# Optimization experiments

Hardware: AMD Instinct MI355X
Metric: run time of the kernel (lower is better)

## Reference

```python
import jax, jax.numpy as jnp
import numpy as np
from jax import lax

B, T, LM, H = 16, 60, 63, 64   # batch, frames, landmark dim, lstm hidden
IMG_H, IMG_W = 240, 320
CONV_FEAT = 252                 # 4 * 7 * 9


def _conv(x, w, b, s):
    # x: [N, Cin, H, W], w: [Cout, Cin, kh, kw], VALID padding, stride s
    y = lax.conv_general_dilated(x, w, (s, s), 'VALID',
                                 dimension_numbers=('NCHW', 'OIHW', 'NCHW'))
    return y + b[None, :, None, None]


def setup_inputs() -> dict:
    key = jax.random.key(0)
    ks = jax.random.split(key, 24)
    s = 0.05
    d = {
        'input': jax.random.normal(ks[0], (B, T, LM), jnp.float32),
        'video': jax.random.uniform(ks[1], (B, T, IMG_H, IMG_W), jnp.float32),
        'W00': jax.random.normal(ks[2], (LM, LM), jnp.float32) * s,
        'b00': jnp.zeros((LM,), jnp.float32),
        'W01': jax.random.normal(ks[3], (64, LM), jnp.float32) * s,
        'b01': jnp.zeros((64,), jnp.float32),
        'Wc0': jax.random.normal(ks[4], (16, 1, 5, 5), jnp.float32) * s,
        'bc0': jnp.zeros((16,), jnp.float32),
        'Wc1': jax.random.normal(ks[5], (16, 16, 5, 5), jnp.float32) * s,
        'bc1': jnp.zeros((16,), jnp.float32),
        'Wc2': jax.random.normal(ks[6], (4, 16, 2, 2), jnp.float32) * s,
        'bc2': jnp.zeros((4,), jnp.float32),
        'Wih': jax.random.normal(ks[7], (4 * H, 64 + CONV_FEAT), jnp.float32) * s,
        'Whh': jax.random.normal(ks[8], (4 * H, H), jnp.float32) * s,
        'bih': jnp.zeros((4 * H,), jnp.float32),
        'bhh': jnp.zeros((4 * H,), jnp.float32),
        'W10': jax.random.normal(ks[9], (32, H), jnp.float32) * s,
        'b10': jnp.zeros((32,), jnp.float32),
        'W11': jax.random.normal(ks[10], (32, 32), jnp.float32) * s,
        'b11': jnp.zeros((32,), jnp.float32),
        'W12': jax.random.normal(ks[11], (256, 32), jnp.float32) * s,
        'b12': jnp.zeros((256,), jnp.float32),
    }
    return d


def reference(input, video, W00, b00, W01, b01, Wc0, bc0, Wc1, bc1, Wc2, bc2,
              Wih, Whh, bih, bhh, W10, b10, W11, b11, W12, b12):
    relu = jax.nn.relu
    # per-frame landmark MLP, vectorized over all frames: [B, T, 64]
    f = relu(jnp.einsum('btl,ml->btm', input, W00) + b00)
    f = relu(jnp.einsum('btl,ml->btm', f, W01) + b01)
    # per-frame conv features, all frames in one batched conv: [B*T, 1, 240, 320]
    v = video.reshape(B * T, 1, IMG_H, IMG_W)
    v = relu(_conv(v, Wc0, bc0, 4))          # [B*T, 16, 59, 79]
    v = relu(_conv(v, Wc1, bc1, 4))          # [B*T, 16, 14, 19]
    v = relu(_conv(v, Wc2, bc2, 2))          # [B*T, 4, 7, 9]
    v = v.reshape(B, T, CONV_FEAT)
    # frame inputs to LSTM: [B, T, 316]
    x = jnp.concatenate([f, v], axis=-1)
    # Torch semantics: LSTM called unbatched with 2D input [B, 316] per frame,
    # so the batch dim is consumed as a sequence; state carries across frames.
    # Total sequence is frame-major: [T, B, 316] -> [T*B, 316].
    seq = x.transpose(1, 0, 2).reshape(T * B, -1)

    def step(carry, xt):
        h, c = carry
        g = xt @ Wih.T + bih + h @ Whh.T + bhh
        i, fg, gg, o = jnp.split(g, 4)
        c = jax.nn.sigmoid(fg) * c + jax.nn.sigmoid(i) * jnp.tanh(gg)
        h = jax.nn.sigmoid(o) * jnp.tanh(c)
        return (h, c), h

    h0 = jnp.zeros((H,), seq.dtype)
    _, hs = lax.scan(step, (h0, h0), seq)    # [T*B, H]
    out = hs[-B:]                            # last frame's full output: [B, H]
    out = relu(out @ W10.T + b10)
    out = relu(out @ W11.T + b11)
    return out @ W12.T + b12                 # [B, 256]
```

## Files before the change

### kernel.cpp

```cpp
#include <hip/hip_runtime.h>
#include <math.h>

#define B_   16
#define T_   60
#define LMD  63
#define IH   240
#define IW   320
#define XDIM 316
#define NSEQ 960
#define NPROD 255

#define G_BYTES   983040

#define P_W0T   0
#define P_BAND  416
#define P_PART  6944
#define P_C1L   8236
#define P_XROW  12760
#define P_X0S   13076
#define P_F1S   13140
#define P_ACT   0
#define P_HSL   512
#define P_M1S   1536
#define P_M2S   1568
#define POOLN   20736

__device__ __forceinline__ float rl(float v, int k) {
    return __uint_as_float((unsigned)__builtin_amdgcn_readlane((int)__float_as_uint(v), k));
}
__device__ __forceinline__ float sig_f(float x) {
    return __builtin_amdgcn_rcpf(1.0f + __expf(-x));
}
__device__ __forceinline__ float tanh_f(float x) {
    return 1.0f - 2.0f * __builtin_amdgcn_rcpf(__expf(2.0f * x) + 1.0f);
}

__device__ __forceinline__ int ensure_rows(const int* flg, int R, int target, int l) {
    while (R < target) {
        int idx = R + l;
        int v = 1;
        if (idx < NSEQ)
            v = __hip_atomic_load(&flg[idx], __ATOMIC_ACQUIRE, __HIP_MEMORY_SCOPE_AGENT);
        unsigned long long m = __ballot(v != 0);
        if (m == 0xFFFFFFFFFFFFFFFFull) { R += 64; continue; }
        int n = (int)(__ffsll((long long)~m) - 1);
        if (n > 0) R += n;
        else __builtin_amdgcn_s_sleep(16);
    }
    return R;
}

__global__ void k_zero(int* __restrict__ flg) {
    int i = blockIdx.x * 256 + threadIdx.x;
    if (i < NSEQ) flg[i] = 0;
}

#define REPW(M) M(0) M(1) M(2) M(3) M(4) M(5) M(6) M(7) \
                M(8) M(9) M(10) M(11) M(12) M(13) M(14) M(15)

__global__ __launch_bounds__(256, 1) void k_all(
        const float* __restrict__ inp,  const float* __restrict__ video,
        const float* __restrict__ W00,  const float* __restrict__ b00,
        const float* __restrict__ W01,  const float* __restrict__ b01,
        const float* __restrict__ Wc0,  const float* __restrict__ bc0,
        const float* __restrict__ Wc1,  const float* __restrict__ bc1,
        const float* __restrict__ Wc2,  const float* __restrict__ bc2,
        const float* __restrict__ Wih,  const float* __restrict__ Whh,
        const float* __restrict__ bih,  const float* __restrict__ bhh,
        const float* __restrict__ W10,  const float* __restrict__ b10,
        const float* __restrict__ W11,  const float* __restrict__ b11,
        const float* __restrict__ W12,  const float* __restrict__ b12,
        float* __restrict__ G, int* __restrict__ flg, float* __restrict__ out)
{
    __shared__ __align__(16) float pool[POOLN];
    int tid = threadIdx.x;

    if (blockIdx.x != 0) {
        float* W0T  = pool + P_W0T;
        float* band = pool + P_BAND;
        float* part = pool + P_PART;
        float* c1L  = pool + P_C1L;
        float* xrow = pool + P_XROW;
        float* x0s  = pool + P_X0S;
        float* f1s  = pool + P_F1S;

        int ch1 = tid & 15, ic = tid >> 4;
        int wave = tid >> 6, lane = tid & 63;
        int d0 = tid / 79, c0c0 = tid % 79;
        int pos1 = tid + 256;
        bool has1 = (pos1 < 395);
        int d1 = has1 ? pos1 / 79 : 0, c0c1 = has1 ? pos1 % 79 : 0;

        for (int i = tid; i < 400; i += 256) { int ch = i / 25, tap = i % 25; W0T[tap * 16 + ch] = Wc0[i]; }
        if (tid < 16) W0T[25 * 16 + tid] = bc0[tid];
        float w1r[25];
#pragma unroll
        for (int tap = 0; tap < 25; ++tap)
            w1r[tap] = Wc1[(ch1 * 16 + ic) * 25 + tap];

        for (int s = (int)blockIdx.x - 1; s < NSEQ; s += NPROD) {
            int t = s >> 4, b = s & 15;
            int bt = b * T_ + t;
            const float* vid = video + (size_t)bt * (IH * IW);

            if (tid < LMD) x0s[tid] = inp[bt * LMD + tid];
            __syncthreads();
            if (tid < LMD) {
                const float* wr = W00 + tid * LMD;
                float a0 = 0.f, a1 = 0.f, a2 = 0.f, a3 = 0.f;
                for (int k = 0; k < 60; k += 4) {
                    a0 += x0s[k + 0] * wr[k + 0];
                    a1 += x0s[k + 1] * wr[k + 1];
                    a2 += x0s[k + 2] * wr[k + 2];
                    a3 += x0s[k + 3] * wr[k + 3];
                }
                a0 += x0s[60] * wr[60]; a1 += x0s[61] * wr[61]; a2 += x0s[62] * wr[62];
                f1s[tid] = fmaxf(((a0 + a1) + (a2 + a3)) + b00[tid], 0.f);
            }
            __syncthreads();
            if (tid < 64) {
                const float* wr = W01 + tid * LMD;
                float a0 = 0.f, a1 = 0.f, a2 = 0.f, a3 = 0.f;
                for (int k = 0; k < 60; k += 4) {
                    a0 += f1s[k + 0] * wr[k + 0];
                    a1 += f1s[k + 1] * wr[k + 1];
                    a2 += f1s[k + 2] * wr[k + 2];
                    a3 += f1s[k + 3] * wr[k + 3];
                }
                a0 += f1s[60] * wr[60]; a1 += f1s[61] * wr[61]; a2 += f1s[62] * wr[62];
                xrow[tid] = fmaxf(((a0 + a1) + (a2 + a3)) + b01[tid], 0.f);
            }

            float PX0[25], PX1[25];
            {
                const float* vb = vid + (4 * d0) * IW + c0c0 * 4;
#pragma unroll
                for (int kr = 0; kr < 5; ++kr) {
                    float4 v = *(const float4*)(vb + kr * IW);
                    PX0[kr*5+0]=v.x; PX0[kr*5+1]=v.y; PX0[kr*5+2]=v.z; PX0[kr*5+3]=v.w;
                    PX0[kr*5+4]=vb[kr*IW+4];
                }
                if (has1) {
                    const float* vc = vid + (4 * d1) * IW + c0c1 * 4;
#pragma unroll
                    for (int kr = 0; kr < 5; ++kr) {
                        float4 v = *(const float4*)(vc + kr * IW);
                        PX1[kr*5+0]=v.x; PX1[kr*5+1]=v.y; PX1[kr*5+2]=v.z; PX1[kr*5+3]=v.w;
                        PX1[kr*5+4]=vc[kr*IW+4];
                    }
                }
            }
            __syncthreads();

            for (int r1 = 0; r1 < 14; ++r1) {
                {
                    float acc[16];
                    {
                        const float4* b4 = (const float4*)&W0T[25 * 16];
                        float4 ba = b4[0], bb = b4[1], bc = b4[2], bd = b4[3];
                        acc[0]=ba.x; acc[1]=ba.y; acc[2]=ba.z; acc[3]=ba.w;
                        acc[4]=bb.x; acc[5]=bb.y; acc[6]=bb.z; acc[7]=bb.w;
                        acc[8]=bc.x; acc[9]=bc.y; acc[10]=bc.z; acc[11]=bc.w;
                        acc[12]=bd.x; acc[13]=bd.y; acc[14]=bd.z; acc[15]=bd.w;
                    }
#pragma unroll
                    for (int tap = 0; tap < 25; ++tap) {
                        float p = PX0[tap];
                        const float4* w4 = (const float4*)&W0T[tap * 16];
                        float4 wa = w4[0], wb = w4[1], wc = w4[2], wd = w4[3];
                        acc[0]+=p*wa.x; acc[1]+=p*wa.y; acc[2]+=p*wa.z; acc[3]+=p*wa.w;
                        acc[4]+=p*wb.x; acc[5]+=p*wb.y; acc[6]+=p*wb.z; acc[7]+=p*wb.w;
                        acc[8]+=p*wc.x; acc[9]+=p*wc.y; acc[10]+=p*wc.z; acc[11]+=p*wc.w;
                        acc[12]+=p*wd.x; acc[13]+=p*wd.y; acc[14]+=p*wd.z; acc[15]+=p*wd.w;
                    }
#pragma unroll
                    for (int ch = 0; ch < 16; ++ch)
                        band[ch * 408 + d0 * 80 + c0c0] = fmaxf(acc[ch], 0.f);
                }
                if (has1) {
                    float acc[16];
                    {
                        const float4* b4 = (const float4*)&W0T[25 * 16];
                        float4 ba = b4[0], bb = b4[1], bc = b4[2], bd = b4[3];
                        acc[0]=ba.x; acc[1]=ba.y; acc[2]=ba.z; acc[3]=ba.w;
                        acc[4]=bb.x; acc[5]=bb.y; acc[6]=bb.z; acc[7]=bb.w;
                        acc[8]=bc.x; acc[9]=bc.y; acc[10]=bc.z; acc[11]=bc.w;
                        acc[12]=bd.x; acc[13]=bd.y; acc[14]=bd.z; acc[15]=bd.w;
                    }
#pragma unroll
                    for (int tap = 0; tap < 25; ++tap) {
                        float p = PX1[tap];
                        const float4* w4 = (const float4*)&W0T[tap * 16];
                        float4 wa = w4[0], wb = w4[1], wc = w4[2], wd = w4[3];
                        acc[0]+=p*wa.x; acc[1]+=p*wa.y; acc[2]+=p*wa.z; acc[3]+=p*wa.w;
                        acc[4]+=p*wb.x; acc[5]+=p*wb.y; acc[6]+=p*wb.z; acc[7]+=p*wb.w;
                        acc[8]+=p*wc.x; acc[9]+=p*wc.y; acc[10]+=p*wc.z; acc[11]+=p*wc.w;
                        acc[12]+=p*wd.x; acc[13]+=p*wd.y; acc[14]+=p*wd.z; acc[15]+=p*wd.w;
                    }
#pragma unroll
                    for (int ch = 0; ch < 16; ++ch)
                        band[ch * 408 + d1 * 80 + c0c1] = fmaxf(acc[ch], 0.f);
                }

                if (r1 + 1 < 14) {
                    const float* vb = vid + (16 * (r1+1) + 4 * d0) * IW + c0c0 * 4;
#pragma unroll
                    for (int kr = 0; kr < 5; ++kr) {
                        float4 v = *(const float4*)(vb + kr * IW);
                        PX0[kr*5+0]=v.x; PX0[kr*5+1]=v.y; PX0[kr*5+2]=v.z; PX0[kr*5+3]=v.w;
                        PX0[kr*5+4]=vb[kr*IW+4];
                    }
                    if (has1) {
                        const float* vc = vid + (16 * (r1+1) + 4 * d1) * IW + c0c1 * 4;
#pragma unroll
                        for (int kr = 0; kr < 5; ++kr) {
                            float4 v = *(const float4*)(vc + kr * IW);
                            PX1[kr*5+0]=v.x; PX1[kr*5+1]=v.y; PX1[kr*5+2]=v.z; PX1[kr*5+3]=v.w;
                            PX1[kr*5+4]=vc[kr*IW+4];
                        }
                    }
                }
                __syncthreads();

                const float* bb0 = &band[ic * 408];
                for (int c1c = 0; c1c < 19; ++c1c) {
                    const float* bb = bb0 + c1c * 4;
                    float a0, a1, a2, a3, a4;
                    {
                        float4 v = *(const float4*)(bb);       float sc = bb[4];
                        a0 = v.x*w1r[0]  + v.y*w1r[1]  + v.z*w1r[2]  + v.w*w1r[3]  + sc*w1r[4];
                    }
                    {
                        float4 v = *(const float4*)(bb + 80);  float sc = bb[84];
                        a1 = v.x*w1r[5]  + v.y*w1r[6]  + v.z*w1r[7]  + v.w*w1r[8]  + sc*w1r[9];
                    }
                    {
                        float4 v = *(const float4*)(bb + 160); float sc = bb[164];
                        a2 = v.x*w1r[10] + v.y*w1r[11] + v.z*w1r[12] + v.w*w1r[13] + sc*w1r[14];
                    }
                    {
                        float4 v = *(const float4*)(bb + 240); float sc = bb[244];
                        a3 = v.x*w1r[15] + v.y*w1r[16] + v.z*w1r[17] + v.w*w1r[18] + sc*w1r[19];
                    }
                    {
                        float4 v = *(const float4*)(bb + 320); float sc = bb[324];
                        a4 = v.x*w1r[20] + v.y*w1r[21] + v.z*w1r[22] + v.w*w1r[23] + sc*w1r[24];
                    }
                    float p = ((a0 + a1) + (a2 + a3)) + a4;
                    p += __shfl_xor(p, 16);
                    p += __shfl_xor(p, 32);
                    if (lane < 16)
                        part[c1c * 68 + wave * 17 + ch1] = p;
                }
                __syncthreads();

                for (int o = tid; o < 304; o += 256) {
                    int c1c = o >> 4, ch = o & 15;
                    const float* pp = &part[c1c * 68 + ch];
                    float v = bc1[ch] + pp[0] + pp[17] + pp[34] + pp[51];
                    c1L[(r1 * 19 + c1c) * 17 + ch] = fmaxf(v, 0.f);
                }
                __syncthreads();
            }

            for (int o = tid; o < 252; o += 256) {
                int ch2 = o / 63, rr = (o / 9) % 7, cc = o % 9;
                float a = bc2[ch2];
                for (int ic2 = 0; ic2 < 16; ++ic2)
                    for (int kr = 0; kr < 2; ++kr)
                        for (int kc = 0; kc < 2; ++kc)
                            a += c1L[((2 * rr + kr) * 19 + 2 * cc + kc) * 17 + ic2] *
                                 Wc2[((ch2 * 16 + ic2) * 2 + kr) * 2 + kc];
                xrow[64 + o] = fmaxf(a, 0.f);
            }
            __syncthreads();

            {
                const float4* x4 = (const float4*)xrow;
                const float4* w4 = (const float4*)(Wih + (size_t)tid * XDIM);
                float a0 = 0.f, a1 = 0.f, a2 = 0.f, a3 = 0.f;
                for (int ko = 0; ko < 79; ++ko) {
                    float4 w = w4[ko], x = x4[ko];
                    a0 += w.x * x.x;
                    a1 += w.y * x.y;
                    a2 += w.z * x.z;
                    a3 += w.w * x.w;
                }
                G[(size_t)s * 256 + tid] = ((a0 + a1) + (a2 + a3)) + (bih[tid] + bhh[tid]);
            }
            __threadfence();
            __syncthreads();
            if (tid == 0)
                __hip_atomic_store(&flg[s], 1, __ATOMIC_RELEASE, __HIP_MEMORY_SCOPE_AGENT);
        }
        return;
    }

    float* act = pool + P_ACT;
    float* hsL = pool + P_HSL;
    float* m1s = pool + P_M1S;
    float* m2s = pool + P_M2S;
    int j = tid;
    int w = j >> 6, l = j & 63;

#define DECLW(n) float4 wv##n;
    REPW(DECLW)
#undef DECLW
    {
        const float4* Wr = (const float4*)(Whh + (size_t)j * 64);
#define LOADW(n) wv##n = Wr[n];
        REPW(LOADW)
#undef LOADW
    }

    float h = 0.f, c = 0.f;
    int R = ensure_rows(flg, 0, 2, l);
    float gc = G[j];
    float gn = G[256 + j];

    for (int tb = 0; tb < NSEQ; tb += 64) {
        int target = tb + 66; if (target > NSEQ) target = NSEQ;
        R = ensure_rows(flg, R, target, l);
        for (int t = tb; t < tb + 64; ++t) {
            float gp = 0.f;
            if (t + 2 < NSEQ)
                gp = G[(size_t)(t + 2) * 256 + j];

            float a0 = gc, a1 = 0.f, a2 = 0.f, a3 = 0.f;
#define GFMA(n) { \
            float h0 = rl(h, 4*(n)+0), h1 = rl(h, 4*(n)+1); \
            float h2 = rl(h, 4*(n)+2), h3 = rl(h, 4*(n)+3); \
            a0 += h0 * wv##n.x; a1 += h1 * wv##n.y; \
            a2 += h2 * wv##n.z; a3 += h3 * wv##n.w; \
        }
            REPW(GFMA)
#undef GFMA
            float g = (a0 + a1) + (a2 + a3);
            float av = (w == 2) ? tanh_f(g) : sig_f(g);
            act[(t & 1) * 256 + j] = av;
            asm volatile("s_waitcnt lgkmcnt(0)\n\ts_barrier" ::: "memory");
            const float* ab = act + (t & 1) * 256;
            float ai = ab[l], af = ab[64 + l], ag = ab[128 + l], ao = ab[192 + l];
            c = af * c + ai * ag;
            h = ao * tanh_f(c);
            if (t >= NSEQ - 16 && w == 0) hsL[(t - (NSEQ - 16)) * 64 + l] = h;
            gc = gn; gn = gp;
        }
    }
    __syncthreads();

    for (int r = 0; r < 16; ++r) {
        if (j < 32) {
            float a = b10[j];
            for (int k = 0; k < 64; ++k) a += hsL[r * 64 + k] * W10[j * 64 + k];
            m1s[j] = fmaxf(a, 0.f);
        }
        __syncthreads();
        if (j < 32) {
            float a = b11[j];
            for (int k = 0; k < 32; ++k) a += m1s[k] * W11[j * 32 + k];
            m2s[j] = fmaxf(a, 0.f);
        }
        __syncthreads();
        {
            float a = b12[j];
            for (int k = 0; k < 32; ++k) a += m2s[k] * W12[j * 32 + k];
            out[r * 256 + j] = a;
        }
        __syncthreads();
    }
}

extern "C" void kernel_launch(void* const* d_in, const int* in_sizes, int n_in,
                              void* d_out, int out_size, void* d_ws, size_t ws_size,
                              hipStream_t stream) {
    const float* inp   = (const float*)d_in[0];
    const float* video = (const float*)d_in[1];
    const float* W00   = (const float*)d_in[2];
    const float* b00   = (const float*)d_in[3];
    const float* W01   = (const float*)d_in[4];
    const float* b01   = (const float*)d_in[5];
    const float* Wc0   = (const float*)d_in[6];
    const float* bc0   = (const float*)d_in[7];
    const float* Wc1   = (const float*)d_in[8];
    const float* bc1   = (const float*)d_in[9];
    const float* Wc2   = (const float*)d_in[10];
    const float* bc2   = (const float*)d_in[11];
    const float* Wih   = (const float*)d_in[12];
    const float* Whh   = (const float*)d_in[13];
    const float* bih   = (const float*)d_in[14];
    const float* bhh   = (const float*)d_in[15];
    const float* W10   = (const float*)d_in[16];
    const float* b10   = (const float*)d_in[17];
    const float* W11   = (const float*)d_in[18];
    const float* b11   = (const float*)d_in[19];
    const float* W12   = (const float*)d_in[20];
    const float* b12   = (const float*)d_in[21];

    float* G  = (float*)d_ws;
    int* flg  = (int*)((char*)d_ws + G_BYTES);

    k_zero<<<4, 256, 0, stream>>>(flg);
    k_all<<<256, 256, 0, stream>>>(inp, video, W00, b00, W01, b01,
                                   Wc0, bc0, Wc1, bc1, Wc2, bc2,
                                   Wih, Whh, bih, bhh,
                                   W10, b10, W11, b11, W12, b12,
                                   G, flg, (float*)d_out);
}
```

Measured before the change: 753.9 us.

## Stage LSTM input-gate rows through double-buffered LDS chunks

Replaces the per-step global load of precomputed gate inputs (prefetched two steps ahead) with chunked prefetch. Each chunk of 32 timesteps is loaded into registers as float4 and written into a double-buffered LDS region, and the recurrence reads from LDS. The aim is to take global-memory latency out of the serial recurrence critical path. The cost is extra registers for staging, a full-block sync per chunk, and coarser waiting on producer flags (32 rows ahead instead of 2), which may delay the start of the recurrence.

```diff
diff --git a/kernel.cpp b/kernel.cpp
--- a/kernel.cpp
+++ b/kernel.cpp
@@ -23,7 +23,11 @@
 #define P_HSL   512
 #define P_M1S   1536
 #define P_M2S   1568
+#define P_GBUF  1600
 #define POOLN   20736
+
+#define CHUNK   32
+#define NCHUNK  30
 
 __device__ __forceinline__ float rl(float v, int k) {
     return __uint_as_float((unsigned)__builtin_amdgcn_readlane((int)__float_as_uint(v), k));
@@ -57,6 +61,7 @@
 
 #define REPW(M) M(0) M(1) M(2) M(3) M(4) M(5) M(6) M(7) \
                 M(8) M(9) M(10) M(11) M(12) M(13) M(14) M(15)
+#define REPS(M) M(0) M(1) M(2) M(3) M(4) M(5) M(6) M(7)
 
 __global__ __launch_bounds__(256, 1) void k_all(
         const float* __restrict__ inp,  const float* __restrict__ video,
@@ -300,6 +305,8 @@
     float* hsL = pool + P_HSL;
     float* m1s = pool + P_M1S;
     float* m2s = pool + P_M2S;
+    float* gbF = pool + P_GBUF;
+    float4* gb4 = (float4*)gbF;
     int j = tid;
     int w = j >> 6, l = j & 63;
 
@@ -313,18 +320,37 @@
 #undef LOADW
     }
 
+#define DECLS(n) float4 st##n;
+    REPS(DECLS)
+#undef DECLS
+    const float4* G4 = (const float4*)G;
+
     float h = 0.f, c = 0.f;
-    int R = ensure_rows(flg, 0, 2, l);
-    float gc = G[j];
-    float gn = G[256 + j];
-
-    for (int tb = 0; tb < NSEQ; tb += 64) {
-        int target = tb + 66; if (target > NSEQ) target = NSEQ;
-        R = ensure_rows(flg, R, target, l);
-        for (int t = tb; t < tb + 64; ++t) {
-            float gp = 0.f;
-            if (t + 2 < NSEQ)
-                gp = G[(size_t)(t + 2) * 256 + j];
+
+    int R = ensure_rows(flg, 0, CHUNK, l);
+#define LOADS0(n) st##n = G4[(n) * 256 + tid];
+    REPS(LOADS0)
+#undef LOADS0
+#define WRITES0(n) gb4[(n) * 256 + tid] = st##n;
+    REPS(WRITES0)
+#undef WRITES0
+    __syncthreads();
+    float gc = gbF[j];
+
+    for (int cb = 0; cb < NCHUNK; ++cb) {
+        int tb = cb * CHUNK;
+        int nb = cb & 1;
+        if (cb + 1 < NCHUNK) {
+            R = ensure_rows(flg, R, tb + 2 * CHUNK, l);
+            const float4* src = G4 + (size_t)(tb + CHUNK) * 64;
+#define LOADS(n) st##n = src[(n) * 256 + tid];
+            REPS(LOADS)
+#undef LOADS
+        }
+        const float* gcur = gbF + nb * 8192;
+        for (int tt = 0; tt < CHUNK; ++tt) {
+            int t = tb + tt;
+            float gnext = (tt + 1 < CHUNK) ? gcur[(tt + 1) * 256 + j] : 0.f;
 
             float a0 = gc, a1 = 0.f, a2 = 0.f, a3 = 0.f;
 #define GFMA(n) { \
@@ -344,8 +370,17 @@
             c = af * c + ai * ag;
             h = ao * tanh_f(c);
             if (t >= NSEQ - 16 && w == 0) hsL[(t - (NSEQ - 16)) * 64 + l] = h;
-            gc = gn; gn = gp;
-        }
+            gc = gnext;
+        }
+        if (cb + 1 < NCHUNK) {
+            float4* dst = gb4 + (nb ^ 1) * 2048;
+#define WRITES(n) dst[(n) * 256 + tid] = st##n;
+            REPS(WRITES)
+#undef WRITES
+        }
+        __syncthreads();
+        if (cb + 1 < NCHUNK)
+            gc = gbF[(nb ^ 1) * 8192 + j];
     }
     __syncthreads();
 
```

Result: no change. 753.5 us (-0.0%).
